# Kernel optimization log

Measured on AMD Instinct MI355X. Metric: run time of the kernel, lower is better.

## Reference

```python
import jax, jax.numpy as jnp
import numpy as np

N = 100000   # nodes
E = 1600000  # edges (avg degree 16)
D = 128      # input feature dim
H = 128      # hidden_dim
O = 64       # output_dim


def setup_inputs() -> dict:
    key = jax.random.key(0)
    ks = jax.random.split(key, 20)
    p = lambda k, shape: (jax.random.normal(k, shape, jnp.float32) * 0.05)
    return {
        "x": jax.random.normal(ks[0], (N, D), jnp.float32),
        "edge_index": jax.random.randint(ks[1], (2, E), 0, N),
        # conv1: bipartite-style -> separate src/dst linears
        "W1s": p(ks[2], (D, H)), "W1d": p(ks[3], (D, H)),
        "a1s": p(ks[4], (H,)), "a1d": p(ks[5], (H,)), "b1": jnp.zeros((H,), jnp.float32),
        # conv2 / conv3: shared linear for src and dst
        "W2": p(ks[6], (H, H)), "a2s": p(ks[7], (H,)), "a2d": p(ks[8], (H,)), "b2": jnp.zeros((H,), jnp.float32),
        "W3": p(ks[9], (H, H)), "a3s": p(ks[10], (H,)), "a3d": p(ks[11], (H,)), "b3": jnp.zeros((H,), jnp.float32),
        # MLP head
        "Wl1": p(ks[12], (H, H)), "bl1": jnp.zeros((H,), jnp.float32),
        "Wl2": p(ks[13], (H, O)), "bl2": jnp.zeros((O,), jnp.float32),
    }


def _gat(x_src, x_dst, Ws, Wd, a_s, a_d, b, src, dst, n):
    """Single-head PyG GATConv (add_self_loops=False)."""
    hs = x_src @ Ws                       # [N, H]
    hd = x_dst @ Wd                       # [N, H]
    # per-edge attention logits: gather node scalars, add, leaky-relu(0.2)
    e = jax.nn.leaky_relu((hs @ a_s)[src] + (hd @ a_d)[dst], 0.2)  # [E]
    # segment softmax over incoming edges of each dst node
    m = jax.ops.segment_max(e, dst, num_segments=n)
    ex = jnp.exp(e - m[dst])
    s = jax.ops.segment_sum(ex, dst, num_segments=n)
    w = ex / (s[dst] + 1e-16)             # [E]
    # weighted scatter-add of source messages
    out = jax.ops.segment_sum(w[:, None] * hs[src], dst, num_segments=n)
    return out + b


def reference(x, edge_index, W1s, W1d, a1s, a1d, b1, W2, a2s, a2d, b2,
              W3, a3s, a3d, b3, Wl1, bl1, Wl2, bl2):
    n = x.shape[0]
    src, dst = edge_index[0], edge_index[1]
    h = jax.nn.relu(_gat(x, x, W1s, W1d, a1s, a1d, b1, src, dst, n))
    h = jax.nn.relu(_gat(h, h, W2, W2, a2s, a2d, b2, src, dst, n))
    h = jax.nn.relu(_gat(h, h, W3, W3, a3s, a3d, b3, src, dst, n))
    h = jax.nn.relu(h @ Wl1 + bl1)
    return h @ Wl2 + bl2
```

## Files before the change

kernel.cpp:

```cpp
#include <hip/hip_runtime.h>
#include <hip/hip_bf16.h>
#include <cstdint>
#include <cstddef>


#define PA_CHUNK 4096
#define BKT_CAP  12288

using short8  = __attribute__((ext_vector_type(8))) short;
using ushort8 = __attribute__((ext_vector_type(8))) unsigned short;
using f32x4   = __attribute__((ext_vector_type(4))) float;

__device__ __forceinline__ ushort f2bf_rne(float f) {
  uint u = __float_as_uint(f);
  u += 0x7FFFu + ((u >> 16) & 1u);
  return (ushort)(u >> 16);
}

__global__ __launch_bounds__(256) void bucket_scatter_kernel(
    const int* __restrict__ src, const int* __restrict__ dst,
    int* __restrict__ bcount, uint* __restrict__ buckets, int E, int NB) {
  __shared__ int  hist[256];
  __shared__ int  base[256];
  __shared__ uint recs[PA_CHUNK];
  __shared__ ushort rb[PA_CHUNK];
  const int t = threadIdx.x;
  const int e0 = blockIdx.x * PA_CHUNK;
  const int nE = min(PA_CHUNK, E - e0);

  for (int i = t; i < 256; i += 256) hist[i] = 0;
  __syncthreads();
  for (int i = t; i < nE; i += 256) {
    int s = src[e0 + i], d = dst[e0 + i];
    int b = d >> 9;
    recs[i] = ((uint)s << 9) | (uint)(d & 511);
    rb[i] = (ushort)b;
    atomicAdd(&hist[b], 1);
  }
  __syncthreads();
  if (t < NB) base[t] = (hist[t] > 0) ? atomicAdd(&bcount[t], hist[t]) : 0;
  __syncthreads();
  for (int i = t; i < 256; i += 256) hist[i] = 0;
  __syncthreads();
  for (int i = t; i < nE; i += 256) {
    int b = rb[i];
    int r = atomicAdd(&hist[b], 1);
    int pos = base[b] + r;
    if (pos < BKT_CAP) buckets[(size_t)b * BKT_CAP + pos] = recs[i];
  }
}

__global__ __launch_bounds__(256) void scan_buckets_kernel(
    const int* __restrict__ bcount, int* __restrict__ bbase, int NB,
    int* __restrict__ row_ptr, int N, int E) {
  __shared__ int s[256];
  int t = threadIdx.x;
  int x = (t < NB) ? bcount[t] : 0;
  s[t] = x;
  __syncthreads();
  #pragma unroll
  for (int off = 1; off < 256; off <<= 1) {
    int v = (t >= off) ? s[t - off] : 0;
    __syncthreads();
    s[t] += v;
    __syncthreads();
  }
  if (t < NB) bbase[t] = s[t] - x;
  if (t == 0) row_ptr[N] = E;
}

__global__ __launch_bounds__(256) void bucket_sort_kernel(
    const uint* __restrict__ buckets, const int* __restrict__ bcount,
    const int* __restrict__ bbase, int* __restrict__ row_ptr,
    int* __restrict__ src_sorted, int N) {
  const int b = blockIdx.x;
  const int t = threadIdx.x;
  __shared__ int h[512], o[512], c[512];
  __shared__ int wsum[4];
  const int cnt = min(bcount[b], BKT_CAP);
  const int gbase = bbase[b];
  const uint* rec = buckets + (size_t)b * BKT_CAP;

  for (int i = t; i < 512; i += 256) { h[i] = 0; c[i] = 0; }
  __syncthreads();
  for (int i = t; i < cnt; i += 256) atomicAdd(&h[rec[i] & 511], 1);
  __syncthreads();

  int a0 = h[2 * t], a1 = h[2 * t + 1];
  int s2 = a0 + a1;
  int lane = t & 63, w = t >> 6;
  int v = s2;
  #pragma unroll
  for (int off = 1; off < 64; off <<= 1) {
    int u = __shfl_up(v, off, 64);
    if (lane >= off) v += u;
  }
  if (lane == 63) wsum[w] = v;
  __syncthreads();
  int woff = 0;
  for (int i = 0; i < w; ++i) woff += wsum[i];
  int excl = (v - s2) + woff;
  o[2 * t]     = excl;
  o[2 * t + 1] = excl + a0;
  __syncthreads();

  for (int i = t; i < 512; i += 256) {
    int node = (b << 9) + i;
    if (node < N) row_ptr[node] = gbase + o[i];
  }
  for (int i = t; i < cnt; i += 256) {
    uint r = rec[i];
    int d9 = r & 511;
    int rk = atomicAdd(&c[d9], 1);
    src_sorted[gbase + o[d9] + rk] = (int)(r >> 9);
  }
}

__device__ __forceinline__ void wprep_one(const float* __restrict__ W,
                                          ushort* __restrict__ Wt, int TN, int local) {
  int n = local % TN;
  int c = local / TN;
  ushort8 o;
  #pragma unroll
  for (int j = 0; j < 8; ++j) o[j] = f2bf_rne(W[(c * 8 + j) * TN + n]);
  *(ushort8*)(Wt + n * 128 + ((c ^ (n & 7)) * 8)) = o;
}

__global__ __launch_bounds__(256) void wprep_all_kernel(
    const float* __restrict__ W1s, const float* __restrict__ W2,
    const float* __restrict__ W3,  const float* __restrict__ Wl1,
    const float* __restrict__ Wl2,
    ushort* __restrict__ Wt1, ushort* __restrict__ Wt2, ushort* __restrict__ Wt3,
    ushort* __restrict__ Wtl1, ushort* __restrict__ Wtl2) {
  int idx = blockIdx.x * 256 + threadIdx.x;
  if (idx < 2048)        wprep_one(W1s, Wt1, 128, idx);
  else if (idx < 4096)   wprep_one(W2,  Wt2, 128, idx - 2048);
  else if (idx < 6144)   wprep_one(W3,  Wt3, 128, idx - 4096);
  else if (idx < 8192)   wprep_one(Wl1, Wtl1, 128, idx - 6144);
  else if (idx < 9216)   wprep_one(Wl2, Wtl2, 64, idx - 8192);
}

template <int TN, bool RELU, bool HASBIAS, bool ABF16, bool OBF16>
__global__ __launch_bounds__(256) void mfma_gemm_kernel(const void* __restrict__ Av,
                                                        const ushort* __restrict__ Wt,
                                                        const float* __restrict__ bias,
                                                        void* __restrict__ Cv, int n) {
  constexpr int WCOLS = TN / 2;
  constexpr int FI = 4;
  constexpr int FJ = WCOLS / 16;
  __shared__ char lds[32768 + TN * 256];
  ushort* sA = (ushort*)lds;
  ushort* sW = (ushort*)(lds + 32768);

  const int t = threadIdx.x;
  const int row0 = blockIdx.x * 128;
  const int lane = t & 63;
  const int wid = t >> 6;
  const int wr = wid >> 1, wc = wid & 1;

  #pragma unroll
  for (int i = 0; i < 8; ++i) {
    int r = i * 16 + (t >> 4);
    int c = t & 15;
    int gr = row0 + r;
    ushort8 o = 0;
    if (ABF16) {
      const ushort* Ab = (const ushort*)Av;
      if (gr < n) o = *(const ushort8*)(Ab + (size_t)gr * 128 + c * 8);
    } else {
      const float* A = (const float*)Av;
      float4 v0 = make_float4(0.f, 0.f, 0.f, 0.f), v1 = v0;
      if (gr < n) {
        const float4* Ar = (const float4*)(A + (size_t)gr * 128);
        v0 = Ar[c * 2];
        v1 = Ar[c * 2 + 1];
      }
      o[0] = f2bf_rne(v0.x); o[1] = f2bf_rne(v0.y); o[2] = f2bf_rne(v0.z); o[3] = f2bf_rne(v0.w);
      o[4] = f2bf_rne(v1.x); o[5] = f2bf_rne(v1.y); o[6] = f2bf_rne(v1.z); o[7] = f2bf_rne(v1.w);
    }
    *(ushort8*)(sA + r * 128 + ((c ^ (r & 7)) * 8)) = o;
  }
  #pragma unroll
  for (int i = 0; i < TN / 16; ++i) {
    int chunk = i * 256 + t;
    *(ushort8*)(sW + chunk * 8) = *(const ushort8*)(Wt + chunk * 8);
  }
  __syncthreads();

  f32x4 acc[FI][FJ] = {};
  const int lm = lane & 15, q = lane >> 4, l7 = lane & 7;

  #pragma unroll
  for (int kk = 0; kk < 4; ++kk) {
    const int cs = kk * 4 + q;
    short8 af[FI], bfr[FJ];
    #pragma unroll
    for (int i = 0; i < FI; ++i) {
      int r = wr * 64 + i * 16 + lm;
      af[i] = *(const short8*)(sA + r * 128 + ((cs ^ l7) * 8));
    }
    #pragma unroll
    for (int j = 0; j < FJ; ++j) {
      int nn = wc * WCOLS + j * 16 + lm;
      bfr[j] = *(const short8*)(sW + nn * 128 + ((cs ^ l7) * 8));
    }
    #pragma unroll
    for (int i = 0; i < FI; ++i)
      #pragma unroll
      for (int j = 0; j < FJ; ++j)
        acc[i][j] = __builtin_amdgcn_mfma_f32_16x16x32_bf16(af[i], bfr[j], acc[i][j], 0, 0, 0);
  }

  #pragma unroll
  for (int i = 0; i < FI; ++i) {
    #pragma unroll
    for (int j = 0; j < FJ; ++j) {
      int gcol = wc * WCOLS + j * 16 + lm;
      float bv = HASBIAS ? bias[gcol] : 0.f;
      #pragma unroll
      for (int r = 0; r < 4; ++r) {
        int grow = row0 + wr * 64 + i * 16 + q * 4 + r;
        if (grow < n) {
          float v = acc[i][j][r] + bv;
          if (RELU) v = fmaxf(v, 0.f);
          if (OBF16) ((ushort*)Cv)[(size_t)grow * TN + gcol] = f2bf_rne(v);
          else       ((float*)Cv)[(size_t)grow * TN + gcol] = v;
        }
      }
    }
  }
}

__global__ void make_v2_kernel(const float* __restrict__ Ws, const float* __restrict__ as_,
                               const float* __restrict__ Wd, const float* __restrict__ ad_,
                               float* __restrict__ vs, float* __restrict__ vd) {
  int gw = blockIdx.x * (blockDim.x >> 6) + (threadIdx.x >> 6);
  int lane = threadIdx.x & 63;
  int d = gw & 127;
  const float* W = (gw < 128) ? Ws : Wd;
  const float* a = (gw < 128) ? as_ : ad_;
  float2 w0 = ((const float2*)(W + d * 128))[lane];
  float2 a0 = ((const float2*)a)[lane];
  float p = w0.x * a0.x + w0.y * a0.y;
  #pragma unroll
  for (int off = 32; off >= 1; off >>= 1) p += __shfl_down(p, off, 64);
  if (lane == 0) ((gw < 128) ? vs : vd)[d] = p;
}

__global__ void alpha_kernel(const float* __restrict__ X, const float* __restrict__ vs,
                             const float* __restrict__ vd, float* __restrict__ as_,
                             float* __restrict__ ad_, int n) {
  int wid = blockIdx.x * (blockDim.x >> 6) + (threadIdx.x >> 6);
  int lane = threadIdx.x & 63;
  if (wid >= n) return;
  float2 xv = ((const float2*)X)[(size_t)wid * 64 + lane];
  float2 v1 = ((const float2*)vs)[lane];
  float2 v2 = ((const float2*)vd)[lane];
  float ps = xv.x * v1.x + xv.y * v1.y;
  float pd = xv.x * v2.x + xv.y * v2.y;
  #pragma unroll
  for (int off = 32; off > 0; off >>= 1) {
    ps += __shfl_down(ps, off, 64);
    pd += __shfl_down(pd, off, 64);
  }
  if (lane == 0) { as_[wid] = ps; ad_[wid] = pd; }
}

__global__ void alphaQ_kernel(const uint* __restrict__ hsb, const float* __restrict__ a_s,
                              const float* __restrict__ a_d, float* __restrict__ as_,
                              float* __restrict__ ad_, int n) {
  int wid = blockIdx.x * (blockDim.x >> 6) + (threadIdx.x >> 6);
  int lane = threadIdx.x & 63;
  if (wid >= n) return;
  uint h = hsb[(size_t)wid * 64 + lane];
  float hx = __uint_as_float(h << 16), hy = __uint_as_float(h & 0xFFFF0000u);
  float2 s2 = ((const float2*)a_s)[lane];
  float2 d2 = ((const float2*)a_d)[lane];
  float ps = hx * s2.x + hy * s2.y;
  float pd = hx * d2.x + hy * d2.y;
  #pragma unroll
  for (int off = 32; off > 0; off >>= 1) {
    ps += __shfl_down(ps, off, 64);
    pd += __shfl_down(pd, off, 64);
  }
  if (lane == 0) { as_[wid] = ps; ad_[wid] = pd; }
}

__global__ void edge_p_kernel(const int* __restrict__ row_ptr, const int* __restrict__ src_sorted,
                              const float* __restrict__ alpha_s, const float* __restrict__ alpha_d,
                              uint2* __restrict__ erec, int n) {
  int wid = blockIdx.x * (blockDim.x >> 6) + (threadIdx.x >> 6);
  int lane = threadIdx.x & 63;
  int node = wid * 4 + (lane >> 4);
  if (node >= n) return;
  int beg = row_ptr[node], end = row_ptr[node + 1];
  float ad = alpha_d[node];
  for (int j = beg + (lane & 15); j < end; j += 16) {
    int u = src_sorted[j];
    float e = alpha_s[u] + ad;
    e = (e > 0.f) ? e : 0.2f * e;
    erec[j] = make_uint2((uint)u, __float_as_uint(__expf(e)));
  }
}

__global__ void gat_aggregate_kernel(const uint2* __restrict__ hs2,
                                     const uint2* __restrict__ erec,
                                     const int* __restrict__ row_ptr,
                                     const float* __restrict__ bias,
                                     uint2* __restrict__ outb, int n) {
  const int t = threadIdx.x;
  const int pairw = blockIdx.x * 4 + (t >> 6);
  const int lane = t & 63;
  const int half = lane >> 5;
  const int sl = lane & 31;
  const int node = pairw * 2 + half;
  const bool active = node < n;
  const int beg = active ? row_ptr[node] : 0;
  const int end = active ? row_ptr[node + 1] : 0;

  float sA = 0.f, sB = 0.f;
  float Ax0 = 0.f, Ay0 = 0.f, Ax1 = 0.f, Ay1 = 0.f;
  float Bx0 = 0.f, By0 = 0.f, Bx1 = 0.f, By1 = 0.f;

  int j = beg;
  for (; j + 4 <= end; j += 4) {
    uint4 eA = *(const uint4*)&erec[j];
    uint4 eB = *(const uint4*)&erec[j + 2];
    uint2 h0 = hs2[(size_t)eA.x * 32 + sl];
    uint2 h1 = hs2[(size_t)eA.z * 32 + sl];
    uint2 h2 = hs2[(size_t)eB.x * 32 + sl];
    uint2 h3 = hs2[(size_t)eB.z * 32 + sl];
    float p0 = __uint_as_float(eA.y), p1 = __uint_as_float(eA.w);
    float p2 = __uint_as_float(eB.y), p3 = __uint_as_float(eB.w);
    sA += p0 + p1;
    sB += p2 + p3;
    Ax0 = fmaf(p0, __uint_as_float(h0.x << 16), Ax0);
    Ay0 = fmaf(p0, __uint_as_float(h0.x & 0xFFFF0000u), Ay0);
    Ax1 = fmaf(p0, __uint_as_float(h0.y << 16), Ax1);
    Ay1 = fmaf(p0, __uint_as_float(h0.y & 0xFFFF0000u), Ay1);
    Bx0 = fmaf(p1, __uint_as_float(h1.x << 16), Bx0);
    By0 = fmaf(p1, __uint_as_float(h1.x & 0xFFFF0000u), By0);
    Bx1 = fmaf(p1, __uint_as_float(h1.y << 16), Bx1);
    By1 = fmaf(p1, __uint_as_float(h1.y & 0xFFFF0000u), By1);
    Ax0 = fmaf(p2, __uint_as_float(h2.x << 16), Ax0);
    Ay0 = fmaf(p2, __uint_as_float(h2.x & 0xFFFF0000u), Ay0);
    Ax1 = fmaf(p2, __uint_as_float(h2.y << 16), Ax1);
    Ay1 = fmaf(p2, __uint_as_float(h2.y & 0xFFFF0000u), Ay1);
    Bx0 = fmaf(p3, __uint_as_float(h3.x << 16), Bx0);
    By0 = fmaf(p3, __uint_as_float(h3.x & 0xFFFF0000u), By0);
    Bx1 = fmaf(p3, __uint_as_float(h3.y << 16), Bx1);
    By1 = fmaf(p3, __uint_as_float(h3.y & 0xFFFF0000u), By1);
  }
  for (; j < end; ++j) {
    uint2 r = erec[j];
    float p = __uint_as_float(r.y);
    uint2 h = hs2[(size_t)r.x * 32 + sl];
    sA += p;
    Ax0 = fmaf(p, __uint_as_float(h.x << 16), Ax0);
    Ay0 = fmaf(p, __uint_as_float(h.x & 0xFFFF0000u), Ay0);
    Ax1 = fmaf(p, __uint_as_float(h.y << 16), Ax1);
    Ay1 = fmaf(p, __uint_as_float(h.y & 0xFFFF0000u), Ay1);
  }

  if (active) {
    float s = sA + sB;
    float inv = 1.f / (s + 1e-16f);
    float4 bv = ((const float4*)bias)[sl];
    float o0 = fmaxf(fmaf(Ax0 + Bx0, inv, bv.x), 0.f);
    float o1 = fmaxf(fmaf(Ay0 + By0, inv, bv.y), 0.f);
    float o2 = fmaxf(fmaf(Ax1 + Bx1, inv, bv.z), 0.f);
    float o3 = fmaxf(fmaf(Ay1 + By1, inv, bv.w), 0.f);
    uint2 pk;
    pk.x = ((uint)f2bf_rne(o1) << 16) | (uint)f2bf_rne(o0);
    pk.y = ((uint)f2bf_rne(o3) << 16) | (uint)f2bf_rne(o2);
    outb[(size_t)node * 32 + sl] = pk;
  }
}

extern "C" void kernel_launch(void* const* d_in, const int* in_sizes, int n_in,
                              void* d_out, int out_size, void* d_ws, size_t ws_size,
                              hipStream_t stream) {
  const float* x     = (const float*)d_in[0];
  const int*   eidx  = (const int*)d_in[1];
  const float* W1s   = (const float*)d_in[2];
  const float* W1d   = (const float*)d_in[3];
  const float* a1s   = (const float*)d_in[4];
  const float* a1d   = (const float*)d_in[5];
  const float* b1    = (const float*)d_in[6];
  const float* W2    = (const float*)d_in[7];
  const float* a2s   = (const float*)d_in[8];
  const float* a2d   = (const float*)d_in[9];
  const float* b2    = (const float*)d_in[10];
  const float* W3    = (const float*)d_in[11];
  const float* a3s   = (const float*)d_in[12];
  const float* a3d   = (const float*)d_in[13];
  const float* b3    = (const float*)d_in[14];
  const float* Wl1   = (const float*)d_in[15];
  const float* bl1   = (const float*)d_in[16];
  const float* Wl2   = (const float*)d_in[17];
  const float* bl2   = (const float*)d_in[18];
  float* out = (float*)d_out;

  const int N = in_sizes[0] / 128;
  const int E = in_sizes[1] / 2;
  const int* src = eidx;
  const int* dst = eidx + E;
  const int NB = (N + 511) >> 9;

  char* base = (char*)d_ws;
  size_t off = 0;
  auto alloc = [&](size_t bytes) -> void* {
    void* p = base + off;
    off += (bytes + 511) & ~(size_t)511;
    return p;
  };
  uint*  Pb       = (uint*)alloc((size_t)N * 128 * 2);
  uint*  Qb       = (uint*)alloc((size_t)N * 128 * 2);
  char*  Q2reg    = (char*)alloc((size_t)N * 128 * 4);
  uint*  buckets  = (uint*)Q2reg;
  uint2* erec     = (uint2*)(Q2reg + ((size_t)24 << 20));
  ushort* Q2b     = (ushort*)Q2reg;
  float* alpha_s  = (float*)alloc((size_t)N * 4);
  float* alpha_d  = (float*)alloc((size_t)N * 4);
  float* vs       = (float*)alloc(128 * 4);
  float* vd       = (float*)alloc(128 * 4);
  int* row_ptr    = (int*)alloc((size_t)(N + 1) * 4);
  int* bcount     = (int*)alloc(256 * 4);
  int* bbase      = (int*)alloc(256 * 4);
  int* src_sorted = (int*)alloc((size_t)E * 4);
  ushort* Wt1     = (ushort*)alloc(128 * 128 * 2);
  ushort* Wt2     = (ushort*)alloc(128 * 128 * 2);
  ushort* Wt3     = (ushort*)alloc(128 * 128 * 2);
  ushort* Wtl1    = (ushort*)alloc(128 * 128 * 2);
  ushort* Wtl2    = (ushort*)alloc(64 * 128 * 2);
  (void)ws_size;

  const int TB = 256;
  const int nwaveblk = (N + 3) / 4;
  const int ggrid = (N + 127) / 128;
  const int pagrid = (E + PA_CHUNK - 1) / PA_CHUNK;
  const int epgrid = (N + 15) / 16;
  const int aggrid = (N + 7) / 8;

  hipMemsetAsync(bcount, 0, 256 * 4, stream);
  bucket_scatter_kernel<<<pagrid, 256, 0, stream>>>(src, dst, bcount, buckets, E, NB);
  scan_buckets_kernel<<<1, 256, 0, stream>>>(bcount, bbase, NB, row_ptr, N, E);
  bucket_sort_kernel<<<NB, 256, 0, stream>>>(buckets, bcount, bbase, row_ptr, src_sorted, N);

  wprep_all_kernel<<<36, 256, 0, stream>>>(W1s, W2, W3, Wl1, Wl2,
                                           Wt1, Wt2, Wt3, Wtl1, Wtl2);

  make_v2_kernel<<<64, 256, 0, stream>>>(W1s, a1s, W1d, a1d, vs, vd);
  alpha_kernel<<<nwaveblk, TB, 0, stream>>>(x, vs, vd, alpha_s, alpha_d, N);
  mfma_gemm_kernel<128, false, false, false, true><<<ggrid, 256, 0, stream>>>(x, Wt1, nullptr, Qb, N);
  edge_p_kernel<<<epgrid, TB, 0, stream>>>(row_ptr, src_sorted, alpha_s, alpha_d, erec, N);
  gat_aggregate_kernel<<<aggrid, TB, 0, stream>>>((const uint2*)Qb, erec, row_ptr, b1, (uint2*)Pb, N);

  mfma_gemm_kernel<128, false, false, true, true><<<ggrid, 256, 0, stream>>>(Pb, Wt2, nullptr, Qb, N);
  alphaQ_kernel<<<nwaveblk, TB, 0, stream>>>(Qb, a2s, a2d, alpha_s, alpha_d, N);
  edge_p_kernel<<<epgrid, TB, 0, stream>>>(row_ptr, src_sorted, alpha_s, alpha_d, erec, N);
  gat_aggregate_kernel<<<aggrid, TB, 0, stream>>>((const uint2*)Qb, erec, row_ptr, b2, (uint2*)Pb, N);

  mfma_gemm_kernel<128, false, false, true, true><<<ggrid, 256, 0, stream>>>(Pb, Wt3, nullptr, Qb, N);
  alphaQ_kernel<<<nwaveblk, TB, 0, stream>>>(Qb, a3s, a3d, alpha_s, alpha_d, N);
  edge_p_kernel<<<epgrid, TB, 0, stream>>>(row_ptr, src_sorted, alpha_s, alpha_d, erec, N);
  gat_aggregate_kernel<<<aggrid, TB, 0, stream>>>((const uint2*)Qb, erec, row_ptr, b3, (uint2*)Pb, N);

  mfma_gemm_kernel<128, true, true, true, true><<<ggrid, 256, 0, stream>>>(Pb, Wtl1, bl1, Q2b, N);
  mfma_gemm_kernel<64, false, true, true, false><<<ggrid, 256, 0, stream>>>(Q2b, Wtl2, bl2, out, N);
}
```

Before: 412.6 us.

## Fuse attention-logit projections into GEMM kernels, removing separate alpha passes

Computes per-node attention scalars alpha_s/alpha_d inside the MFMA GEMM epilogue by dotting the fp32 accumulators with the attention vectors and reducing across lanes and through LDS. For layer 1, alpha_d is computed in the GEMM's A-load prologue from fp32 x against a precomputed W1d·a1d vector. This removes the alpha_kernel and alphaQ_kernel launches, which each reread the full node feature matrix. In exchange it adds an extra LDS sync and shuffle reductions to the GEMMs, and alpha now comes from unrounded fp32 accumulators rather than bf16 outputs.

```diff
diff --git a/kernel.cpp b/kernel.cpp
--- a/kernel.cpp
+++ b/kernel.cpp
@@ -140,11 +140,28 @@
   else if (idx < 9216)   wprep_one(Wl2, Wtl2, 64, idx - 8192);
 }
 
-template <int TN, bool RELU, bool HASBIAS, bool ABF16, bool OBF16>
+__global__ __launch_bounds__(256) void make_vd_kernel(const float* __restrict__ Wd,
+                                                      const float* __restrict__ ad_,
+                                                      float* __restrict__ vd) {
+  int gw = blockIdx.x * 4 + (threadIdx.x >> 6);
+  int lane = threadIdx.x & 63;
+  float2 w0 = ((const float2*)(Wd + gw * 128))[lane];
+  float2 a0 = ((const float2*)ad_)[lane];
+  float p = w0.x * a0.x + w0.y * a0.y;
+  #pragma unroll
+  for (int off = 32; off >= 1; off >>= 1) p += __shfl_down(p, off, 64);
+  if (lane == 0) vd[gw] = p;
+}
+
+template <int TN, bool RELU, bool HASBIAS, bool ABF16, bool OBF16, int ALPHA>
 __global__ __launch_bounds__(256) void mfma_gemm_kernel(const void* __restrict__ Av,
                                                         const ushort* __restrict__ Wt,
                                                         const float* __restrict__ bias,
-                                                        void* __restrict__ Cv, int n) {
+                                                        void* __restrict__ Cv, int n,
+                                                        const float* __restrict__ asv,
+                                                        const float* __restrict__ adv,
+                                                        float* __restrict__ alpha_s,
+                                                        float* __restrict__ alpha_d) {
   constexpr int WCOLS = TN / 2;
   constexpr int FI = 4;
   constexpr int FJ = WCOLS / 16;
@@ -157,6 +174,12 @@
   const int lane = t & 63;
   const int wid = t >> 6;
   const int wr = wid >> 1, wc = wid & 1;
+
+  float4 vd0, vd1;
+  if constexpr (ALPHA == 2) {
+    vd0 = ((const float4*)adv)[(t & 15) * 2];
+    vd1 = ((const float4*)adv)[(t & 15) * 2 + 1];
+  }
 
   #pragma unroll
   for (int i = 0; i < 8; ++i) {
@@ -175,6 +198,15 @@
         v0 = Ar[c * 2];
         v1 = Ar[c * 2 + 1];
       }
+      if constexpr (ALPHA == 2) {
+        float pd = v0.x * vd0.x + v0.y * vd0.y + v0.z * vd0.z + v0.w * vd0.w
+                 + v1.x * vd1.x + v1.y * vd1.y + v1.z * vd1.z + v1.w * vd1.w;
+        pd += __shfl_xor(pd, 1, 64);
+        pd += __shfl_xor(pd, 2, 64);
+        pd += __shfl_xor(pd, 4, 64);
+        pd += __shfl_xor(pd, 8, 64);
+        if ((t & 15) == 0 && gr < n) alpha_d[gr] = pd;
+      }
       o[0] = f2bf_rne(v0.x); o[1] = f2bf_rne(v0.y); o[2] = f2bf_rne(v0.z); o[3] = f2bf_rne(v0.w);
       o[4] = f2bf_rne(v1.x); o[5] = f2bf_rne(v1.y); o[6] = f2bf_rne(v1.z); o[7] = f2bf_rne(v1.w);
     }
@@ -229,61 +261,50 @@
       }
     }
   }
-}
-
-__global__ void make_v2_kernel(const float* __restrict__ Ws, const float* __restrict__ as_,
-                               const float* __restrict__ Wd, const float* __restrict__ ad_,
-                               float* __restrict__ vs, float* __restrict__ vd) {
-  int gw = blockIdx.x * (blockDim.x >> 6) + (threadIdx.x >> 6);
-  int lane = threadIdx.x & 63;
-  int d = gw & 127;
-  const float* W = (gw < 128) ? Ws : Wd;
-  const float* a = (gw < 128) ? as_ : ad_;
-  float2 w0 = ((const float2*)(W + d * 128))[lane];
-  float2 a0 = ((const float2*)a)[lane];
-  float p = w0.x * a0.x + w0.y * a0.y;
-  #pragma unroll
-  for (int off = 32; off >= 1; off >>= 1) p += __shfl_down(p, off, 64);
-  if (lane == 0) ((gw < 128) ? vs : vd)[d] = p;
-}
-
-__global__ void alpha_kernel(const float* __restrict__ X, const float* __restrict__ vs,
-                             const float* __restrict__ vd, float* __restrict__ as_,
-                             float* __restrict__ ad_, int n) {
-  int wid = blockIdx.x * (blockDim.x >> 6) + (threadIdx.x >> 6);
-  int lane = threadIdx.x & 63;
-  if (wid >= n) return;
-  float2 xv = ((const float2*)X)[(size_t)wid * 64 + lane];
-  float2 v1 = ((const float2*)vs)[lane];
-  float2 v2 = ((const float2*)vd)[lane];
-  float ps = xv.x * v1.x + xv.y * v1.y;
-  float pd = xv.x * v2.x + xv.y * v2.y;
-  #pragma unroll
-  for (int off = 32; off > 0; off >>= 1) {
-    ps += __shfl_down(ps, off, 64);
-    pd += __shfl_down(pd, off, 64);
-  }
-  if (lane == 0) { as_[wid] = ps; ad_[wid] = pd; }
-}
-
-__global__ void alphaQ_kernel(const uint* __restrict__ hsb, const float* __restrict__ a_s,
-                              const float* __restrict__ a_d, float* __restrict__ as_,
-                              float* __restrict__ ad_, int n) {
-  int wid = blockIdx.x * (blockDim.x >> 6) + (threadIdx.x >> 6);
-  int lane = threadIdx.x & 63;
-  if (wid >= n) return;
-  uint h = hsb[(size_t)wid * 64 + lane];
-  float hx = __uint_as_float(h << 16), hy = __uint_as_float(h & 0xFFFF0000u);
-  float2 s2 = ((const float2*)a_s)[lane];
-  float2 d2 = ((const float2*)a_d)[lane];
-  float ps = hx * s2.x + hy * s2.y;
-  float pd = hx * d2.x + hy * d2.y;
-  #pragma unroll
-  for (int off = 32; off > 0; off >>= 1) {
-    ps += __shfl_down(ps, off, 64);
-    pd += __shfl_down(pd, off, 64);
-  }
-  if (lane == 0) { as_[wid] = ps; ad_[wid] = pd; }
+
+  if constexpr (ALPHA >= 1) {
+    __syncthreads();
+    float* srs = (float*)lds;
+    float* srd = (float*)lds + 256;
+    float asl[FJ], adl[FJ];
+    #pragma unroll
+    for (int j = 0; j < FJ; ++j) {
+      int gcol = wc * WCOLS + j * 16 + lm;
+      asl[j] = asv[gcol];
+      if constexpr (ALPHA == 1) adl[j] = adv[gcol];
+    }
+    #pragma unroll
+    for (int i = 0; i < FI; ++i) {
+      #pragma unroll
+      for (int r = 0; r < 4; ++r) {
+        float ps = 0.f, pdp = 0.f;
+        #pragma unroll
+        for (int j = 0; j < FJ; ++j) {
+          ps = fmaf(acc[i][j][r], asl[j], ps);
+          if constexpr (ALPHA == 1) pdp = fmaf(acc[i][j][r], adl[j], pdp);
+        }
+        ps += __shfl_xor(ps, 1, 64); ps += __shfl_xor(ps, 2, 64);
+        ps += __shfl_xor(ps, 4, 64); ps += __shfl_xor(ps, 8, 64);
+        if constexpr (ALPHA == 1) {
+          pdp += __shfl_xor(pdp, 1, 64); pdp += __shfl_xor(pdp, 2, 64);
+          pdp += __shfl_xor(pdp, 4, 64); pdp += __shfl_xor(pdp, 8, 64);
+        }
+        if (lm == 0) {
+          int rl = wr * 64 + i * 16 + q * 4 + r;
+          srs[rl * 2 + wc] = ps;
+          if constexpr (ALPHA == 1) srd[rl * 2 + wc] = pdp;
+        }
+      }
+    }
+    __syncthreads();
+    if (t < 128) {
+      int grow = row0 + t;
+      if (grow < n) {
+        alpha_s[grow] = srs[t * 2] + srs[t * 2 + 1];
+        if constexpr (ALPHA == 1) alpha_d[grow] = srd[t * 2] + srd[t * 2 + 1];
+      }
+    }
+  }
 }
 
 __global__ void edge_p_kernel(const int* __restrict__ row_ptr, const int* __restrict__ src_sorted,
@@ -422,7 +443,6 @@
   ushort* Q2b     = (ushort*)Q2reg;
   float* alpha_s  = (float*)alloc((size_t)N * 4);
   float* alpha_d  = (float*)alloc((size_t)N * 4);
-  float* vs       = (float*)alloc(128 * 4);
   float* vd       = (float*)alloc(128 * 4);
   int* row_ptr    = (int*)alloc((size_t)(N + 1) * 4);
   int* bcount     = (int*)alloc(256 * 4);
@@ -436,7 +456,6 @@
   (void)ws_size;
 
   const int TB = 256;
-  const int nwaveblk = (N + 3) / 4;
   const int ggrid = (N + 127) / 128;
   const int pagrid = (E + PA_CHUNK - 1) / PA_CHUNK;
   const int epgrid = (N + 15) / 16;
@@ -449,23 +468,25 @@
 
   wprep_all_kernel<<<36, 256, 0, stream>>>(W1s, W2, W3, Wl1, Wl2,
                                            Wt1, Wt2, Wt3, Wtl1, Wtl2);
-
-  make_v2_kernel<<<64, 256, 0, stream>>>(W1s, a1s, W1d, a1d, vs, vd);
-  alpha_kernel<<<nwaveblk, TB, 0, stream>>>(x, vs, vd, alpha_s, alpha_d, N);
-  mfma_gemm_kernel<128, false, false, false, true><<<ggrid, 256, 0, stream>>>(x, Wt1, nullptr, Qb, N);
+  make_vd_kernel<<<32, 256, 0, stream>>>(W1d, a1d, vd);
+
+  mfma_gemm_kernel<128, false, false, false, true, 2><<<ggrid, 256, 0, stream>>>(
+      x, Wt1, nullptr, Qb, N, a1s, vd, alpha_s, alpha_d);
   edge_p_kernel<<<epgrid, TB, 0, stream>>>(row_ptr, src_sorted, alpha_s, alpha_d, erec, N);
   gat_aggregate_kernel<<<aggrid, TB, 0, stream>>>((const uint2*)Qb, erec, row_ptr, b1, (uint2*)Pb, N);
 
-  mfma_gemm_kernel<128, false, false, true, true><<<ggrid, 256, 0, stream>>>(Pb, Wt2, nullptr, Qb, N);
-  alphaQ_kernel<<<nwaveblk, TB, 0, stream>>>(Qb, a2s, a2d, alpha_s, alpha_d, N);
+  mfma_gemm_kernel<128, false, false, true, true, 1><<<ggrid, 256, 0, stream>>>(
+      Pb, Wt2, nullptr, Qb, N, a2s, a2d, alpha_s, alpha_d);
   edge_p_kernel<<<epgrid, TB, 0, stream>>>(row_ptr, src_sorted, alpha_s, alpha_d, erec, N);
   gat_aggregate_kernel<<<aggrid, TB, 0, stream>>>((const uint2*)Qb, erec, row_ptr, b2, (uint2*)Pb, N);
 
-  mfma_gemm_kernel<128, false, false, true, true><<<ggrid, 256, 0, stream>>>(Pb, Wt3, nullptr, Qb, N);
-  alphaQ_kernel<<<nwaveblk, TB, 0, stream>>>(Qb, a3s, a3d, alpha_s, alpha_d, N);
+  mfma_gemm_kernel<128, false, false, true, true, 1><<<ggrid, 256, 0, stream>>>(
+      Pb, Wt3, nullptr, Qb, N, a3s, a3d, alpha_s, alpha_d);
   edge_p_kernel<<<epgrid, TB, 0, stream>>>(row_ptr, src_sorted, alpha_s, alpha_d, erec, N);
   gat_aggregate_kernel<<<aggrid, TB, 0, stream>>>((const uint2*)Qb, erec, row_ptr, b3, (uint2*)Pb, N);
 
-  mfma_gemm_kernel<128, true, true, true, true><<<ggrid, 256, 0, stream>>>(Pb, Wtl1, bl1, Q2b, N);
-  mfma_gemm_kernel<64, false, true, true, false><<<ggrid, 256, 0, stream>>>(Q2b, Wtl2, bl2, out, N);
-}
+  mfma_gemm_kernel<128, true, true, true, true, 0><<<ggrid, 256, 0, stream>>>(
+      Pb, Wtl1, bl1, Q2b, N, nullptr, nullptr, nullptr, nullptr);
+  mfma_gemm_kernel<64, false, true, true, false, 0><<<ggrid, 256, 0, stream>>>(
+      Q2b, Wtl2, bl2, out, N, nullptr, nullptr, nullptr, nullptr);
+}
```

Result: faster. 385.2 us (-6.6%).
